# Kernel tuning notes

Hardware: AMD Instinct MI355X
Metric: run time of the kernel (lower is better)

Reference implementation:

```python
import jax, jax.numpy as jnp
import numpy as np

B = 16384       # batch of Monte-Carlo paths
NSTEPS = 32     # time discretization N
H = 128         # hidden width of sub-networks
L = 1.0         # sphere radius l
T1 = 1.0
T0 = 0.0
DT = float((T1 - T0) / NSTEPS)


def _mlp(n, x, W1, b1, W2, b2):
    # sub-network on concat([N, X]): (B,1)+(B,3) -> (B,out)
    inp = jnp.concatenate([n, x], axis=-1)
    h = jnp.tanh(inp @ W1.T + b1)
    return h @ W2.T + b2


def _forward(process_N, process_X, discrete_t, delta_B,
             rW1, rb1, rW2, rb2, gW1, gb1, gW2, gb2, jW1, jb1, jW2, jb2):
    eye = jnp.eye(3, dtype=process_X.dtype)
    alpha = 0.3 * jax.nn.sigmoid(0.1 * process_N)    # birth intensity, (N+1,B,1)
    beta = 0.2 * jax.nn.sigmoid(-0.1 * process_N)    # death intensity, (N+1,B,1)
    u0 = _mlp(process_N[0], process_X[0], rW1, rb1, rW2, rb2)  # result net, (B,1)

    def step(u, xs):
        (Ni, Xi, Np1, ti, dB, ai, bi,
         gW1i, gb1i, gW2i, gb2i, jW1i, jb1i, jW2i, jb2i) = xs
        grad_u = _mlp(Ni, Xi, gW1i, gb1i, gW2i, gb2i)           # (B,3)
        outer = Xi[:, :, None] * Xi[:, None, :] / (L * L)       # (B,3,3)
        sigma = jnp.swapaxes(eye - outer, -2, -1)               # sigma0(X)^T
        T_inv = eye + outer
        k = jnp.sqrt(2.0 / (1.0 + 0.1 * Ni * Ni)) / L           # sqrt(2 D(N))/l, (B,1)
        kg = k * grad_u
        grad_bmm = jnp.einsum('bi,bij,bjk,bk->b', kg, T_inv, sigma, dB)[:, None]
        ui = _mlp(Ni, Xi, jW1i, jb1i, jW2i, jb2i)
        uip = _mlp(Ni + 1.0, Xi, jW1i, jb1i, jW2i, jb2i)
        uim = _mlp(Ni - 1.0, Xi, jW1i, jb1i, jW2i, jb2i)
        dp = uip - ui
        dm = uim - ui
        f = -0.05 * u + 0.05 * jnp.sum(grad_u * Xi, -1, keepdims=True) / L + 0.01 * ti
        u = u + grad_bmm - (ai * dp + bi * dm) * DT - f * DT
        dN = jnp.round(Np1 - Ni)
        u = u + jnp.where(dN > 0, dp, 0.0) + jnp.where(dN < 0, dm, 0.0)
        return u, None

    xs = (process_N[:-1], process_X[:-1], process_N[1:], discrete_t[:-1], delta_B,
          alpha[:-1], beta[:-1], gW1, gb1, gW2, gb2, jW1, jb1, jW2, jb2)
    u, _ = jax.lax.scan(step, u0, xs)
    g = 0.1 * process_N[-1] + jnp.cos(process_X[-1][:, :1])    # terminal condition
    return u, g


def setup_inputs():
    key = jax.random.key(0)
    ks = jax.random.split(key, 16)
    # integer-valued jump process N_t (kept float32), increments in {-1,0,1}
    n0 = jax.random.randint(ks[0], (1, B, 1), 5, 15).astype(jnp.float32)
    jumps = jax.random.randint(ks[1], (NSTEPS, B, 1), -1, 2).astype(jnp.float32)
    process_N = jnp.concatenate([n0, n0 + jnp.cumsum(jumps, axis=0)], axis=0)
    # spatial process on the sphere of radius L
    xr = jax.random.normal(ks[2], (NSTEPS + 1, B, 3), dtype=jnp.float32)
    process_X = L * xr / jnp.linalg.norm(xr, axis=-1, keepdims=True)
    discrete_t = jnp.linspace(T0, T1, NSTEPS + 1, dtype=jnp.float32)
    delta_B = jax.random.normal(ks[3], (NSTEPS, B, 3), dtype=jnp.float32) * float(np.sqrt(DT))

    def lin(k, shape, fan_in):
        return jax.random.normal(k, shape, dtype=jnp.float32) / float(np.sqrt(fan_in))

    rW1 = lin(ks[4], (H, 4), 4);           rb1 = jnp.zeros((H,), jnp.float32)
    rW2 = lin(ks[5], (1, H), H);           rb2 = jnp.zeros((1,), jnp.float32)
    gW1 = lin(ks[6], (NSTEPS, H, 4), 4);   gb1 = jnp.zeros((NSTEPS, H), jnp.float32)
    gW2 = lin(ks[7], (NSTEPS, 3, H), H);   gb2 = jnp.zeros((NSTEPS, 3), jnp.float32)
    jW1 = lin(ks[8], (NSTEPS, H, 4), 4);   jb1 = jnp.zeros((NSTEPS, H), jnp.float32)
    jW2 = lin(ks[9], (NSTEPS, 1, H), H);   jb2 = jnp.zeros((NSTEPS, 1), jnp.float32)
    return dict(process_N=process_N, process_X=process_X, discrete_t=discrete_t,
                delta_B=delta_B, rW1=rW1, rb1=rb1, rW2=rW2, rb2=rb2,
                gW1=gW1, gb1=gb1, gW2=gW2, gb2=gb2,
                jW1=jW1, jb1=jb1, jW2=jW2, jb2=jb2)


def reference(process_N, process_X, discrete_t, delta_B,
              rW1, rb1, rW2, rb2, gW1, gb1, gW2, gb2, jW1, jb1, jW2, jb2):
    return _forward(process_N, process_X, discrete_t, delta_B,
                    rW1, rb1, rW2, rb2, gW1, gb1, gW2, gb2, jW1, jb1, jW2, jb2)
```

## Files before the change

### kernel.cpp

```cpp
#include <hip/hip_runtime.h>
#include <math.h>

#define BB 16384
#define NSTEPS 32
#define HH 128
#define DTF (1.0f/32.0f)
#define SCALE 2.88539008177792681f
#define LOG2E 1.44269504088896340f

typedef float v2f __attribute__((ext_vector_type(2)));
typedef float v8f __attribute__((ext_vector_type(8)));

__device__ __forceinline__ v2f pk_fma(v2f a, v2f b, v2f c) {
    return __builtin_elementwise_fma(a, b, c);
}

__device__ __forceinline__ float fexp2(float x) {
#if __has_builtin(__builtin_amdgcn_exp2f)
    return __builtin_amdgcn_exp2f(x);
#else
    float r; asm("v_exp_f32 %0, %1" : "=v"(r) : "v"(x)); return r;
#endif
}
__device__ __forceinline__ float frcp(float x) {
#if __has_builtin(__builtin_amdgcn_rcpf)
    return __builtin_amdgcn_rcpf(x);
#else
    float r; asm("v_rcp_f32 %0, %1" : "=v"(r) : "v"(x)); return r;
#endif
}
__device__ __forceinline__ float frsq(float x) {
#if __has_builtin(__builtin_amdgcn_rsqf)
    return __builtin_amdgcn_rsqf(x);
#else
    float r; asm("v_rsq_f32 %0, %1" : "=v"(r) : "v"(x)); return r;
#endif
}

__global__ __launch_bounds__(HH) void xform_kernel(
    const float* __restrict__ gW1, const float* __restrict__ gb1,
    const float* __restrict__ gW2, const float* __restrict__ gb2,
    const float* __restrict__ jW1, const float* __restrict__ jb1,
    const float* __restrict__ jW2,
    float* __restrict__ recA, float* __restrict__ G)
{
    const int i = blockIdx.x;
    const int j = threadIdx.x;
    float* r = recA + ((size_t)(i*HH + j)) * 16;

    const float* gw = gW1 + (size_t)(i*HH + j)*4;
    const float* jw = jW1 + (size_t)(i*HH + j)*4;
    float jw0 = jw[0];
    r[0] = SCALE*gw[0]; r[1] = SCALE*jw0;
    r[2] = SCALE*gw[1]; r[3] = SCALE*jw[1];
    r[4] = SCALE*gw[2]; r[5] = SCALE*jw[2];
    r[6] = SCALE*gw[3]; r[7] = SCALE*jw[3];
    r[8] = SCALE*gb1[i*HH + j];
    r[9] = SCALE*jb1[i*HH + j];
    float g20 = gW2[i*3*HH + 0*HH + j];
    float g21 = gW2[i*3*HH + 1*HH + j];
    float g22 = gW2[i*3*HH + 2*HH + j];
    r[10] = -2.0f*g20; r[11] = -2.0f*g21;
    r[12] = -2.0f*g22; r[13] = -2.0f*jW2[i*HH + j];
    r[14] = exp2f( SCALE*jw0);
    r[15] = exp2f(-SCALE*jw0);

    __shared__ float sh[3*HH];
    sh[0*HH + j] = g20; sh[1*HH + j] = g21; sh[2*HH + j] = g22;
    __syncthreads();
    if (j < 3) {
        float s = gb2[i*3 + j];
        for (int t = 0; t < HH; ++t) s += sh[j*HH + t];
        G[i*4 + j] = s;
    }
}

__global__ __launch_bounds__(256) void step_kernel(
    const float* __restrict__ N, const float* __restrict__ X,
    const float* __restrict__ T, const float* __restrict__ dB,
    const float* __restrict__ recA, const float* __restrict__ G,
    float* __restrict__ C)
{
    const int i  = blockIdx.x >> 6;
    const int b  = ((blockIdx.x & 63) << 8) | threadIdx.x;
    const int ib = i*BB + b;

    const float Ni  = N[ib];
    const float Np1 = N[ib + BB];
    const float x0 = X[(size_t)ib*3 + 0], x1 = X[(size_t)ib*3 + 1], x2 = X[(size_t)ib*3 + 2];
    const float d0 = dB[(size_t)ib*3 + 0], d1 = dB[(size_t)ib*3 + 1], d2 = dB[(size_t)ib*3 + 2];
    const float ti = T[i];

    const v8f* rec8 = (const v8f*)(recA + (size_t)i*HH*16);

    const v2f Niv = {Ni, Ni};
    const v2f x0v = {x0, x0};
    const v2f x1v = {x1, x1};
    const v2f x2v = {x2, x2};
    const v2f one = {1.0f, 1.0f};

    v2f ga01 = {0.f, 0.f};
    v2f g2a0 = {0.f, 0.f};
    v2f aPM  = {0.f, 0.f};

#pragma unroll 4
    for (int j = 0; j < HH; ++j) {
        const v8f A = rec8[2*j + 0];
        const v8f Bv = rec8[2*j + 1];

        v2f acc = {Bv[0], Bv[1]};
        acc = pk_fma((v2f){A[0], A[1]}, Niv, acc);
        acc = pk_fma((v2f){A[2], A[3]}, x0v, acc);
        acc = pk_fma((v2f){A[4], A[5]}, x1v, acc);
        acc = pk_fma((v2f){A[6], A[7]}, x2v, acc);

        const float eg = fexp2(acc[0]);
        const float eb = fexp2(acc[1]);

        v2f t01 = (v2f){eg, eb} + one;
        v2f tpm = pk_fma((v2f){eb, eb}, (v2f){Bv[6], Bv[7]}, one);

        const float rg = frcp(t01[0]);
        const float r0 = frcp(t01[1]);
        const float rp = frcp(tpm[0]);
        const float rm = frcp(tpm[1]);

        ga01 = pk_fma((v2f){Bv[2], Bv[3]}, (v2f){rg, rg}, ga01);
        g2a0 = pk_fma((v2f){Bv[4], Bv[5]}, (v2f){rg, r0}, g2a0);
        aPM  = pk_fma((v2f){Bv[5], Bv[5]}, (v2f){rp, rm}, aPM);
    }

    const float g0 = G[i*4 + 0] + ga01[0];
    const float g1 = G[i*4 + 1] + ga01[1];
    const float g2 = G[i*4 + 2] + g2a0[0];
    const float a0 = g2a0[1];
    const float aP = aPM[0];
    const float aM = aPM[1];

    const float gdx = g0*x0 + g1*x1 + g2*x2;
    const float ss  = x0*x0 + x1*x1 + x2*x2;
    const float gdB = g0*d0 + g1*d1 + g2*d2;
    const float xdB = x0*d0 + x1*d1 + x2*d2;

    const float k = 1.41421356237309505f * frsq(fmaf(0.1f*Ni, Ni, 1.0f));
    const float grad_bmm = k * (gdB - ss*gdx*xdB);

    const float dp = aP - a0;
    const float dm = aM - a0;

    const float sig = frcp(1.0f + fexp2(-0.1f*LOG2E*Ni));
    const float alpha = 0.3f*sig;
    const float beta  = 0.2f - 0.2f*sig;

    const float dd = Np1 - Ni;
    const float jump = (dd > 0.5f) ? dp : ((dd < -0.5f) ? dm : 0.0f);

    const float c = grad_bmm - (alpha*dp + beta*dm)*DTF
                  - 0.05f*DTF*gdx - 0.01f*DTF*ti + jump;
    C[ib] = c;
}

__global__ __launch_bounds__(256) void final_kernel(
    const float* __restrict__ N, const float* __restrict__ X,
    const float* __restrict__ rW1, const float* __restrict__ rb1,
    const float* __restrict__ rW2, const float* __restrict__ rb2,
    const float* __restrict__ C, float* __restrict__ out)
{
    const int gid = blockIdx.x*256 + threadIdx.x;
    const int b = gid >> 3;
    const int p = gid & 7;

    const float n0 = N[b];
    const float x0 = X[(size_t)b*3 + 0], x1 = X[(size_t)b*3 + 1], x2 = X[(size_t)b*3 + 2];

    float accw = 0.f, accr = 0.f;
#pragma unroll
    for (int t = 0; t < 16; ++t) {
        const int j = p*16 + t;
        float pre = fmaf(rW1[j*4+0], n0, fmaf(rW1[j*4+1], x0,
                    fmaf(rW1[j*4+2], x1, fmaf(rW1[j*4+3], x2, rb1[j]))));
        float r  = frcp(1.0f + fexp2(SCALE*pre));
        float w2 = rW2[j];
        accw += w2;
        accr = fmaf(w2, r, accr);
    }
    accw += __shfl_down(accw, 4, 8);  accr += __shfl_down(accr, 4, 8);
    accw += __shfl_down(accw, 2, 8);  accr += __shfl_down(accr, 2, 8);
    accw += __shfl_down(accw, 1, 8);  accr += __shfl_down(accr, 1, 8);

    if (p == 0) {
        float u = rb2[0] + accw - 2.0f*accr;

        const float sfac = 1.0f + 0.05f*DTF;
#pragma unroll
        for (int i = 0; i < NSTEPS; ++i)
            u = fmaf(u, sfac, C[(size_t)i*BB + b]);
        out[b] = u;

        const int ib = NSTEPS*BB + b;
        out[BB + b] = fmaf(0.1f, N[ib], __cosf(X[(size_t)ib*3]));
    }
}

extern "C" void kernel_launch(void* const* d_in, const int* in_sizes, int n_in,
                              void* d_out, int out_size, void* d_ws, size_t ws_size,
                              hipStream_t stream)
{
    const float* N   = (const float*)d_in[0];
    const float* X   = (const float*)d_in[1];
    const float* T   = (const float*)d_in[2];
    const float* dB  = (const float*)d_in[3];
    const float* rW1 = (const float*)d_in[4];
    const float* rb1 = (const float*)d_in[5];
    const float* rW2 = (const float*)d_in[6];
    const float* rb2 = (const float*)d_in[7];
    const float* gW1 = (const float*)d_in[8];
    const float* gb1 = (const float*)d_in[9];
    const float* gW2 = (const float*)d_in[10];
    const float* gb2 = (const float*)d_in[11];
    const float* jW1 = (const float*)d_in[12];
    const float* jb1 = (const float*)d_in[13];
    const float* jW2 = (const float*)d_in[14];

    float* ws   = (float*)d_ws;
    float* C    = ws;
    float* recA = ws + (size_t)NSTEPS*BB;
    float* G    = recA + (size_t)NSTEPS*HH*16;
    float* out  = (float*)d_out;

    xform_kernel<<<NSTEPS, HH, 0, stream>>>(gW1, gb1, gW2, gb2, jW1, jb1, jW2, recA, G);
    step_kernel<<<NSTEPS*64, 256, 0, stream>>>(N, X, T, dB, recA, G, C);
    final_kernel<<<BB*8/256, 256, 0, stream>>>(N, X, rW1, rb1, rW2, rb2, C, out);
}
```

Measured before the change: 69.80 us.

## Split hidden units across thread halves, use packed Newton reciprocal approximation

The step kernel now gives each batch element two threads, each covering half of the 128 hidden units, and combines the partial sums through shared memory. This doubles the number of threads, which is meant to improve latency hiding. The four hardware v_rcp calls per hidden unit become a packed bit-trick reciprocal seed with one Newton step, and the exponent argument is clamped to 25 to keep that approximation in range. This approximation is less accurate than the hardware reciprocal. The final kernel also spreads the result-net hidden units over 16 lanes instead of 8.

```diff
diff --git a/kernel.cpp b/kernel.cpp
--- a/kernel.cpp
+++ b/kernel.cpp
@@ -10,9 +10,18 @@
 
 typedef float v2f __attribute__((ext_vector_type(2)));
 typedef float v8f __attribute__((ext_vector_type(8)));
+typedef unsigned int v2u __attribute__((ext_vector_type(2)));
 
 __device__ __forceinline__ v2f pk_fma(v2f a, v2f b, v2f c) {
     return __builtin_elementwise_fma(a, b, c);
+}
+
+__device__ __forceinline__ v2f pk_rcp1(v2f x) {
+    v2u xb; __builtin_memcpy(&xb, &x, 8);
+    v2u yb = (v2u){0x7EF311C3u, 0x7EF311C3u} - xb;
+    v2f y;  __builtin_memcpy(&y, &yb, 8);
+    v2f u = pk_fma(-x, y, (v2f){2.0f, 2.0f});
+    return y * u;
 }
 
 __device__ __forceinline__ float fexp2(float x) {
@@ -81,38 +90,41 @@
     const float* __restrict__ recA, const float* __restrict__ G,
     float* __restrict__ C)
 {
-    const int i  = blockIdx.x >> 6;
-    const int b  = ((blockIdx.x & 63) << 8) | threadIdx.x;
-    const int ib = i*BB + b;
-
-    const float Ni  = N[ib];
-    const float Np1 = N[ib + BB];
+    const int tid  = threadIdx.x;
+    const int i    = blockIdx.x >> 7;
+    const int bblk = blockIdx.x & 127;
+    const int bl   = tid & 127;
+    const int jh   = tid >> 7;
+    const int b    = bblk*128 + bl;
+    const int ib   = i*BB + b;
+
+    const float Ni = N[ib];
     const float x0 = X[(size_t)ib*3 + 0], x1 = X[(size_t)ib*3 + 1], x2 = X[(size_t)ib*3 + 2];
-    const float d0 = dB[(size_t)ib*3 + 0], d1 = dB[(size_t)ib*3 + 1], d2 = dB[(size_t)ib*3 + 2];
-    const float ti = T[i];
-
-    const v8f* rec8 = (const v8f*)(recA + (size_t)i*HH*16);
+
+    const v8f* rec8 = (const v8f*)(recA + (size_t)i*HH*16) + (size_t)jh*128;
 
     const v2f Niv = {Ni, Ni};
     const v2f x0v = {x0, x0};
     const v2f x1v = {x1, x1};
     const v2f x2v = {x2, x2};
     const v2f one = {1.0f, 1.0f};
+    const v2f c25 = {25.0f, 25.0f};
 
     v2f ga01 = {0.f, 0.f};
     v2f g2a0 = {0.f, 0.f};
     v2f aPM  = {0.f, 0.f};
 
 #pragma unroll 4
-    for (int j = 0; j < HH; ++j) {
-        const v8f A = rec8[2*j + 0];
-        const v8f Bv = rec8[2*j + 1];
+    for (int t = 0; t < 64; ++t) {
+        const v8f A  = rec8[2*t + 0];
+        const v8f Bv = rec8[2*t + 1];
 
         v2f acc = {Bv[0], Bv[1]};
         acc = pk_fma((v2f){A[0], A[1]}, Niv, acc);
         acc = pk_fma((v2f){A[2], A[3]}, x0v, acc);
         acc = pk_fma((v2f){A[4], A[5]}, x1v, acc);
         acc = pk_fma((v2f){A[6], A[7]}, x2v, acc);
+        acc = __builtin_elementwise_min(acc, c25);
 
         const float eg = fexp2(acc[0]);
         const float eb = fexp2(acc[1]);
@@ -120,44 +132,54 @@
         v2f t01 = (v2f){eg, eb} + one;
         v2f tpm = pk_fma((v2f){eb, eb}, (v2f){Bv[6], Bv[7]}, one);
 
-        const float rg = frcp(t01[0]);
-        const float r0 = frcp(t01[1]);
-        const float rp = frcp(tpm[0]);
-        const float rm = frcp(tpm[1]);
-
-        ga01 = pk_fma((v2f){Bv[2], Bv[3]}, (v2f){rg, rg}, ga01);
-        g2a0 = pk_fma((v2f){Bv[4], Bv[5]}, (v2f){rg, r0}, g2a0);
-        aPM  = pk_fma((v2f){Bv[5], Bv[5]}, (v2f){rp, rm}, aPM);
-    }
-
-    const float g0 = G[i*4 + 0] + ga01[0];
-    const float g1 = G[i*4 + 1] + ga01[1];
-    const float g2 = G[i*4 + 2] + g2a0[0];
-    const float a0 = g2a0[1];
-    const float aP = aPM[0];
-    const float aM = aPM[1];
-
-    const float gdx = g0*x0 + g1*x1 + g2*x2;
-    const float ss  = x0*x0 + x1*x1 + x2*x2;
-    const float gdB = g0*d0 + g1*d1 + g2*d2;
-    const float xdB = x0*d0 + x1*d1 + x2*d2;
-
-    const float k = 1.41421356237309505f * frsq(fmaf(0.1f*Ni, Ni, 1.0f));
-    const float grad_bmm = k * (gdB - ss*gdx*xdB);
-
-    const float dp = aP - a0;
-    const float dm = aM - a0;
-
-    const float sig = frcp(1.0f + fexp2(-0.1f*LOG2E*Ni));
-    const float alpha = 0.3f*sig;
-    const float beta  = 0.2f - 0.2f*sig;
-
-    const float dd = Np1 - Ni;
-    const float jump = (dd > 0.5f) ? dp : ((dd < -0.5f) ? dm : 0.0f);
-
-    const float c = grad_bmm - (alpha*dp + beta*dm)*DTF
-                  - 0.05f*DTF*gdx - 0.01f*DTF*ti + jump;
-    C[ib] = c;
+        v2f r01 = pk_rcp1(t01);
+        v2f rpm = pk_rcp1(tpm);
+
+        ga01 = pk_fma((v2f){Bv[2], Bv[3]}, (v2f){r01[0], r01[0]}, ga01);
+        g2a0 = pk_fma((v2f){Bv[4], Bv[5]}, r01, g2a0);
+        aPM  = pk_fma((v2f){Bv[5], Bv[5]}, rpm, aPM);
+    }
+
+    __shared__ float sh[6][128];
+    if (jh) {
+        sh[0][bl] = ga01[0]; sh[1][bl] = ga01[1]; sh[2][bl] = g2a0[0];
+        sh[3][bl] = g2a0[1]; sh[4][bl] = aPM[0];  sh[5][bl] = aPM[1];
+    }
+    __syncthreads();
+    if (!jh) {
+        const float g0 = G[i*4 + 0] + ga01[0] + sh[0][bl];
+        const float g1 = G[i*4 + 1] + ga01[1] + sh[1][bl];
+        const float g2 = G[i*4 + 2] + g2a0[0] + sh[2][bl];
+        const float a0 = g2a0[1] + sh[3][bl];
+        const float aP = aPM[0]  + sh[4][bl];
+        const float aM = aPM[1]  + sh[5][bl];
+
+        const float Np1 = N[ib + BB];
+        const float d0 = dB[(size_t)ib*3 + 0], d1 = dB[(size_t)ib*3 + 1], d2 = dB[(size_t)ib*3 + 2];
+        const float ti = T[i];
+
+        const float gdx = g0*x0 + g1*x1 + g2*x2;
+        const float ss  = x0*x0 + x1*x1 + x2*x2;
+        const float gdB = g0*d0 + g1*d1 + g2*d2;
+        const float xdB = x0*d0 + x1*d1 + x2*d2;
+
+        const float k = 1.41421356237309505f * frsq(fmaf(0.1f*Ni, Ni, 1.0f));
+        const float grad_bmm = k * (gdB - ss*gdx*xdB);
+
+        const float dp = aP - a0;
+        const float dm = aM - a0;
+
+        const float sig = frcp(1.0f + fexp2(-0.1f*LOG2E*Ni));
+        const float alpha = 0.3f*sig;
+        const float beta  = 0.2f - 0.2f*sig;
+
+        const float dd = Np1 - Ni;
+        const float jump = (dd > 0.5f) ? dp : ((dd < -0.5f) ? dm : 0.0f);
+
+        const float c = grad_bmm - (alpha*dp + beta*dm)*DTF
+                      - 0.05f*DTF*gdx - 0.01f*DTF*ti + jump;
+        C[ib] = c;
+    }
 }
 
 __global__ __launch_bounds__(256) void final_kernel(
@@ -167,16 +189,16 @@
     const float* __restrict__ C, float* __restrict__ out)
 {
     const int gid = blockIdx.x*256 + threadIdx.x;
-    const int b = gid >> 3;
-    const int p = gid & 7;
+    const int b = gid >> 4;
+    const int p = gid & 15;
 
     const float n0 = N[b];
     const float x0 = X[(size_t)b*3 + 0], x1 = X[(size_t)b*3 + 1], x2 = X[(size_t)b*3 + 2];
 
     float accw = 0.f, accr = 0.f;
 #pragma unroll
-    for (int t = 0; t < 16; ++t) {
-        const int j = p*16 + t;
+    for (int t = 0; t < 8; ++t) {
+        const int j = p*8 + t;
         float pre = fmaf(rW1[j*4+0], n0, fmaf(rW1[j*4+1], x0,
                     fmaf(rW1[j*4+2], x1, fmaf(rW1[j*4+3], x2, rb1[j]))));
         float r  = frcp(1.0f + fexp2(SCALE*pre));
@@ -184,9 +206,10 @@
         accw += w2;
         accr = fmaf(w2, r, accr);
     }
-    accw += __shfl_down(accw, 4, 8);  accr += __shfl_down(accr, 4, 8);
-    accw += __shfl_down(accw, 2, 8);  accr += __shfl_down(accr, 2, 8);
-    accw += __shfl_down(accw, 1, 8);  accr += __shfl_down(accr, 1, 8);
+    accw += __shfl_down(accw, 8, 16);  accr += __shfl_down(accr, 8, 16);
+    accw += __shfl_down(accw, 4, 16);  accr += __shfl_down(accr, 4, 16);
+    accw += __shfl_down(accw, 2, 16);  accr += __shfl_down(accr, 2, 16);
+    accw += __shfl_down(accw, 1, 16);  accr += __shfl_down(accr, 1, 16);
 
     if (p == 0) {
         float u = rb2[0] + accw - 2.0f*accr;
@@ -229,6 +252,6 @@
     float* out  = (float*)d_out;
 
     xform_kernel<<<NSTEPS, HH, 0, stream>>>(gW1, gb1, gW2, gb2, jW1, jb1, jW2, recA, G);
-    step_kernel<<<NSTEPS*64, 256, 0, stream>>>(N, X, T, dB, recA, G, C);
-    final_kernel<<<BB*8/256, 256, 0, stream>>>(N, X, rW1, rb1, rW2, rb2, C, out);
-}
+    step_kernel<<<NSTEPS*(BB/128), 256, 0, stream>>>(N, X, T, dB, recA, G, C);
+    final_kernel<<<BB*16/256, 256, 0, stream>>>(N, X, rW1, rb1, rW2, rb2, C, out);
+}
```

New measurement: 138.5 us. +98.5%, slower.
